# Kernel tuning notes

Hardware: AMD Instinct MI355X
Metric: run time of the kernel (lower is better)

Reference implementation:

```python
import jax, jax.numpy as jnp
import numpy as np

N = 50000       # nodes
E = 400000      # edges (avg degree 8)
IN, HID, OUT, ED = 128, 256, 128, 64
EXP = 2          # GENConv MLP expansion
EPS_MSG = 1e-7   # GENConv eps added to relu(msg)
EPS_BN = 1e-5    # BatchNorm eps
EPS_SM = 1e-16   # PyG softmax denominator eps


def _lin(key, fi, fo):
    w = jax.random.normal(key, (fi, fo), jnp.float32) / np.float32(np.sqrt(fi))
    return w, jnp.zeros((fo,), jnp.float32)


def _layer_params(key, fi, fo, ed):
    ks = jax.random.split(key, 5)
    Wsrc, bsrc = _lin(ks[0], fi, fo)
    Wdst, bdst = _lin(ks[1], fi, fo)
    We, be = _lin(ks[2], ed, fo)
    W1, b1 = _lin(ks[3], fo, fo * EXP)
    W2, b2 = _lin(ks[4], fo * EXP, fo)
    g = jnp.ones((fo * EXP,), jnp.float32)   # BN gamma
    bt = jnp.zeros((fo * EXP,), jnp.float32) # BN beta
    return dict(Wsrc=Wsrc, bsrc=bsrc, Wdst=Wdst, bdst=bdst, We=We, be=be,
                W1=W1, b1=b1, g=g, bt=bt, W2=W2, b2=b2)


def setup_inputs() -> dict:
    key = jax.random.key(0)
    k0, k1, k2, k3, k4 = jax.random.split(key, 5)
    inp = {
        'x': jax.random.normal(k0, (N, IN), jnp.float32),
        'edge_index': jax.random.randint(k1, (2, E), 0, N, jnp.int32),
        'edge_attr': jax.random.normal(k2, (E, ED), jnp.float32),
    }
    for pref, p in (('l1_', _layer_params(k3, IN, HID, ED)),
                    ('l2_', _layer_params(k4, HID, OUT, ED))):
        for n, v in p.items():
            inp[pref + n] = v
    return inp


def _genconv(x, src, dst, ea, Wsrc, bsrc, Wdst, bdst, We, be, W1, b1, g, bt, W2, b2):
    n = x.shape[0]
    h = x @ Wsrc + bsrc                          # [N, F] lin_src
    e = ea @ We + be                             # [E, F] lin_edge
    msg = jax.nn.relu(h[src] + e) + EPS_MSG      # [E, F] message
    # softmax aggregation over destination nodes (t = 1.0)
    mx = jax.ops.segment_max(msg, dst, num_segments=n)
    ex = jnp.exp(msg - mx[dst])
    den = jax.ops.segment_sum(ex, dst, num_segments=n)
    alpha = ex / (den[dst] + EPS_SM)
    agg = jax.ops.segment_sum(alpha * msg, dst, num_segments=n)  # [N, F]
    out = agg + (x @ Wdst + bdst)                # residual lin_dst
    # MLP: Linear -> BatchNorm(train stats) -> ReLU -> Linear
    h1 = out @ W1 + b1                           # [N, 2F]
    mu = h1.mean(0)
    var = h1.var(0)
    h1 = (h1 - mu) * jax.lax.rsqrt(var + EPS_BN) * g + bt
    return jax.nn.relu(h1) @ W2 + b2


def reference(x, edge_index, edge_attr,
              l1_Wsrc, l1_bsrc, l1_Wdst, l1_bdst, l1_We, l1_be,
              l1_W1, l1_b1, l1_g, l1_bt, l1_W2, l1_b2,
              l2_Wsrc, l2_bsrc, l2_Wdst, l2_bdst, l2_We, l2_be,
              l2_W1, l2_b1, l2_g, l2_bt, l2_W2, l2_b2):
    src, dst = edge_index[0], edge_index[1]
    h = _genconv(x, src, dst, edge_attr,
                 l1_Wsrc, l1_bsrc, l1_Wdst, l1_bdst, l1_We, l1_be,
                 l1_W1, l1_b1, l1_g, l1_bt, l1_W2, l1_b2)
    h = jax.nn.relu(h)
    return _genconv(h, src, dst, edge_attr,
                    l2_Wsrc, l2_bsrc, l2_Wdst, l2_bdst, l2_We, l2_be,
                    l2_W1, l2_b1, l2_g, l2_bt, l2_W2, l2_b2)
```

## Files before the change

### kernel.cpp

```cpp
#include <hip/hip_runtime.h>

typedef unsigned short u16;
typedef unsigned int u32;
typedef __attribute__((ext_vector_type(8))) short sv8;
typedef __attribute__((ext_vector_type(4))) float fv4;
typedef __attribute__((ext_vector_type(4))) unsigned short us4;
typedef __attribute__((ext_vector_type(2))) unsigned short us2;

__device__ __forceinline__ u16 f2b(float x) {
    union { float f; u32 u; } a; a.f = x;
    u32 r = a.u + 0x7FFFu + ((a.u >> 16) & 1u);
    return (u16)(r >> 16);
}
__device__ __forceinline__ float b2f(u16 h) {
    union { u32 u; float f; } a; a.u = ((u32)h) << 16;
    return a.f;
}

__device__ __forceinline__ void gll16(const void* g, void* l) {
    __builtin_amdgcn_global_load_lds((__attribute__((address_space(1))) void*)g,
                                     (__attribute__((address_space(3))) void*)l,
                                     16, 0, 0);
}

template<bool AF32, bool AAFF, int EPI, bool STATS>
__global__ __launch_bounds__(256) void k_gemm(
    const void* __restrict__ Aptr, const u16* __restrict__ Wt,
    const float* __restrict__ bias, void* __restrict__ Cptr,
    int M, int K, int F,
    const float* __restrict__ sc, const float* __restrict__ sh,
    float* __restrict__ sums, float* __restrict__ sumsq)
{
    __shared__ u16 As[64][36];
    __shared__ u16 Bs[64][36];
    __shared__ u16 Cs[64][68];
    const int t = threadIdx.x, w = t >> 6, l = t & 63;
    const int n0 = blockIdx.x * 64, m0 = blockIdx.y * 64;
    const int arow = t >> 2, acol = (t & 3) << 3;
    const size_t gr = (size_t)(m0 + arow < M ? m0 + arow : M - 1);

    fv4 acc[4] = {};

    for (int k0 = 0; k0 < K; k0 += 32) {
        sv8 av;
        if constexpr (AF32) {
            const float* Af = (const float*)Aptr;
            fv4 u0 = *(const fv4*)(Af + gr * K + k0 + acol);
            fv4 u1 = *(const fv4*)(Af + gr * K + k0 + acol + 4);
            #pragma unroll
            for (int j = 0; j < 4; ++j) { av[j] = (short)f2b(u0[j]); av[j + 4] = (short)f2b(u1[j]); }
        } else if constexpr (AAFF) {
            sv8 v = *(const sv8*)((const u16*)Aptr + gr * K + k0 + acol);
            fv4 c0 = *(const fv4*)(sc + k0 + acol), c1 = *(const fv4*)(sc + k0 + acol + 4);
            fv4 d0 = *(const fv4*)(sh + k0 + acol), d1 = *(const fv4*)(sh + k0 + acol + 4);
            #pragma unroll
            for (int j = 0; j < 4; ++j) {
                av[j]     = (short)f2b(fmaxf(b2f((u16)v[j])     * c0[j] + d0[j], 0.f));
                av[j + 4] = (short)f2b(fmaxf(b2f((u16)v[j + 4]) * c1[j] + d1[j], 0.f));
            }
        } else {
            av = *(const sv8*)((const u16*)Aptr + gr * K + k0 + acol);
        }
        *(sv8*)&As[arow][acol] = av;
        *(sv8*)&Bs[arow][acol] = *(const sv8*)(Wt + (size_t)(n0 + arow) * K + k0 + acol);
        __syncthreads();

        sv8 a = *(const sv8*)&As[(w << 4) + (l & 15)][(l >> 4) << 3];
        #pragma unroll
        for (int ct = 0; ct < 4; ++ct) {
            sv8 b = *(const sv8*)&Bs[(ct << 4) + (l & 15)][(l >> 4) << 3];
            acc[ct] = __builtin_amdgcn_mfma_f32_16x16x32_bf16(a, b, acc[ct], 0, 0, 0);
        }
        __syncthreads();
    }

    const int lr0 = (w << 4) + ((l >> 4) << 2);
    #pragma unroll
    for (int ct = 0; ct < 4; ++ct) {
        const int col = (ct << 4) + (l & 15);
        const float bv = bias[n0 + col];
        float s = 0.f, s2 = 0.f;
        #pragma unroll
        for (int r = 0; r < 4; ++r) {
            const int lrow = lr0 + r;
            const bool valid = (m0 + lrow) < M;
            float v = acc[ct][r] + bv;
            if constexpr (STATS) { if (valid) { s += v; s2 += v * v; } }
            if constexpr (EPI == 1) v = fmaxf(v, 0.f);
            if constexpr (EPI == 3) {
                if (valid) ((float*)Cptr)[(size_t)(m0 + lrow) * F + n0 + col] = v;
            } else {
                Cs[lrow][col] = f2b(v);
            }
        }
        if constexpr (STATS) {
            s  += __shfl_xor(s, 16);  s  += __shfl_xor(s, 32);
            s2 += __shfl_xor(s2, 16); s2 += __shfl_xor(s2, 32);
            if (l < 16) { unsafeAtomicAdd(&sums[n0 + col], s); unsafeAtomicAdd(&sumsq[n0 + col], s2); }
        }
    }
    if constexpr (EPI != 3) {
        __syncthreads();
        const int lrow = t >> 2, c0 = (t & 3) << 4;
        if (m0 + lrow < M) {
            u16* Cb = (u16*)Cptr + (size_t)(m0 + lrow) * F + n0 + c0;
            *(sv8*)Cb       = *(const sv8*)&Cs[lrow][c0];
            *(sv8*)(Cb + 8) = *(const sv8*)&Cs[lrow][c0 + 8];
        }
    }
}

template<int FN>
__global__ __launch_bounds__(256) void k_egemm(
    const u16* __restrict__ Ab, const u16* __restrict__ Wt,
    const float* __restrict__ bias, u16* __restrict__ Cbuf)
{
    __shared__ u16 smem[4096 + FN * 64];
    u16* As = smem;
    u16* Bs = smem + 4096;
    u16* Cs = Bs;
    const int t = threadIdx.x, w = t >> 6, l = t & 63;
    const int m0 = blockIdx.x * 64;

    #pragma unroll
    for (int i = 0; i < 2; ++i) {
        int slot = ((w * 2 + i) << 6) + l;
        int row = slot >> 3, g = (slot & 7) ^ (row & 7);
        gll16(Ab + (size_t)(m0 + row) * 64 + g * 8, As + ((w * 2 + i) << 6) * 8);
    }
    constexpr int BISS = FN / 32;
    #pragma unroll
    for (int i = 0; i < BISS; ++i) {
        int slot = ((w * BISS + i) << 6) + l;
        int row = slot >> 3, g = (slot & 7) ^ (row & 7);
        gll16(Wt + (size_t)row * 64 + g * 8, Bs + ((w * BISS + i) << 6) * 8);
    }
    __syncthreads();

    const int Arow = (w << 4) + (l & 15);
    const int g0 = l >> 4;
    sv8 a0 = *(const sv8*)&As[(Arow * 8 + ((g0)     ^ (Arow & 7))) * 8];
    sv8 a1 = *(const sv8*)&As[(Arow * 8 + ((g0 + 4) ^ (Arow & 7))) * 8];
    fv4 acc[FN / 16] = {};
    #pragma unroll
    for (int ct = 0; ct < FN / 16; ++ct) {
        int Brow = (ct << 4) + (l & 15);
        sv8 b0 = *(const sv8*)&Bs[(Brow * 8 + ((g0)     ^ (Brow & 7))) * 8];
        sv8 b1 = *(const sv8*)&Bs[(Brow * 8 + ((g0 + 4) ^ (Brow & 7))) * 8];
        acc[ct] = __builtin_amdgcn_mfma_f32_16x16x32_bf16(a0, b0, acc[ct], 0, 0, 0);
        acc[ct] = __builtin_amdgcn_mfma_f32_16x16x32_bf16(a1, b1, acc[ct], 0, 0, 0);
    }
    __syncthreads();

    #pragma unroll
    for (int ct = 0; ct < FN / 16; ++ct) {
        const int col = (ct << 4) + (l & 15);
        const float bv = bias[col];
        #pragma unroll
        for (int r = 0; r < 4; ++r) {
            const int row = (w << 4) + ((l >> 4) << 2) + r;
            int my = (int)f2b(acc[ct][r] + bv);
            int ot = __shfl_xor(my, 1);
            if (!(l & 1)) {
                u32 dw = ((u32)my & 0xFFFFu) | ((u32)ot << 16);
                int gp = (col >> 3) ^ (row & 7);
                ((u32*)Cs)[(row * FN + gp * 8 + (col & 7)) >> 1] = dw;
            }
        }
    }
    __syncthreads();

    const int row = t >> 2;
    #pragma unroll
    for (int i = 0; i < FN / 32; ++i) {
        int g = (t & 3) * (FN / 32) + i;
        int gp = (g & ~7) | ((g & 7) ^ (row & 7));
        sv8 v = *(const sv8*)&Cs[row * FN + gp * 8];
        *(sv8*)(Cbuf + (size_t)(m0 + row) * FN + g * 8) = v;
    }
}

__global__ void k_hist(const int* __restrict__ dst, int* __restrict__ counts, int E) {
    int i = blockIdx.x * 256 + threadIdx.x;
    if (i < E) atomicAdd(&counts[dst[i]], 1);
}

__global__ __launch_bounds__(256) void k_psum(const int* __restrict__ counts,
                                              int* __restrict__ bsum, int n) {
    int i = blockIdx.x * 256 + threadIdx.x;
    int v = (i < n) ? counts[i] : 0;
    #pragma unroll
    for (int o = 1; o < 64; o <<= 1) v += __shfl_xor(v, o);
    __shared__ int ws[4];
    if ((threadIdx.x & 63) == 0) ws[threadIdx.x >> 6] = v;
    __syncthreads();
    if (threadIdx.x == 0) bsum[blockIdx.x] = ws[0] + ws[1] + ws[2] + ws[3];
}

__global__ __launch_bounds__(256) void k_bscan(const int* __restrict__ bsum,
                                               int* __restrict__ boff, int nb) {
    __shared__ int sm[256];
    int t = threadIdx.x;
    int v = (t < nb) ? bsum[t] : 0;
    sm[t] = v; __syncthreads();
    #pragma unroll
    for (int o = 1; o < 256; o <<= 1) {
        int u = (t >= o) ? sm[t - o] : 0;
        __syncthreads();
        sm[t] += u;
        __syncthreads();
    }
    if (t < nb) boff[t] = sm[t] - v;
}

__global__ __launch_bounds__(256) void k_windp(const int* __restrict__ counts,
                                               const int* __restrict__ boff,
                                               int* __restrict__ indptr,
                                               int* __restrict__ cursors, int n) {
    __shared__ int sm[256];
    const int t = threadIdx.x, i = blockIdx.x * 256 + t;
    int v = (i < n) ? counts[i] : 0;
    sm[t] = v; __syncthreads();
    #pragma unroll
    for (int o = 1; o < 256; o <<= 1) {
        int u = (t >= o) ? sm[t - o] : 0;
        __syncthreads();
        sm[t] += u;
        __syncthreads();
    }
    int excl = sm[t] - v + boff[blockIdx.x];
    if (i < n) { indptr[i] = excl; cursors[i] = excl; }
    if (i == n - 1) indptr[n] = excl + v;
}

__global__ void k_scatter(const int* __restrict__ dst, const int* __restrict__ src,
                          int* __restrict__ cursors, int* __restrict__ perm,
                          int* __restrict__ srcp, int E) {
    int i = blockIdx.x * 256 + threadIdx.x;
    if (i < E) {
        int p = atomicAdd(&cursors[dst[i]], 1);
        perm[p] = i;
        srcp[p] = src[i];
    }
}

__global__ __launch_bounds__(256) void k_permea(
    const float* __restrict__ ea, const int* __restrict__ perm,
    u16* __restrict__ eab)
{
    const int t = threadIdx.x;
    const int p = blockIdx.x * 64 + (t >> 2);
    const int q = t & 3;
    const float* srcr = ea + (size_t)perm[p] * 64 + q * 16;
    u16 o[16];
    #pragma unroll
    for (int i = 0; i < 4; ++i) {
        fv4 u = *(const fv4*)(srcr + i * 4);
        o[i * 4 + 0] = f2b(u[0]); o[i * 4 + 1] = f2b(u[1]);
        o[i * 4 + 2] = f2b(u[2]); o[i * 4 + 3] = f2b(u[3]);
    }
    *(sv8*)(eab + (size_t)p * 64 + q * 16)     = *(sv8*)&o[0];
    *(sv8*)(eab + (size_t)p * 64 + q * 16 + 8) = *(sv8*)&o[8];
}

template<int F, int VPT>
__global__ __launch_bounds__(256) void k_agg(
    const u16* __restrict__ e, const u16* __restrict__ hhd,
    const int* __restrict__ srcp, const int* __restrict__ indptr,
    u16* __restrict__ out, int N)
{
    const int nid = blockIdx.x * 4 + (threadIdx.x >> 6);
    if (nid >= N) return;
    const int c0 = (threadIdx.x & 63) * VPT;
    const int S = 2 * F;
    const int p0 = indptr[nid], p1 = indptr[nid + 1];
    float den[VPT] = {}, num[VPT] = {};
    for (int p = p0; p < p1; ++p) {
        const int s = srcp[p];
        u16 ev[VPT], hv[VPT];
        if constexpr (VPT == 4) {
            *(us4*)ev = *(const us4*)&e[(size_t)p * F + c0];
            *(us4*)hv = *(const us4*)&hhd[(size_t)s * S + c0];
        } else {
            *(us2*)ev = *(const us2*)&e[(size_t)p * F + c0];
            *(us2*)hv = *(const us2*)&hhd[(size_t)s * S + c0];
        }
        #pragma unroll
        for (int j = 0; j < VPT; ++j) {
            float x = fmaxf(b2f(ev[j]) + b2f(hv[j]), 0.f) + 1e-7f;
            float ex = __expf(x);
            den[j] += ex;
            num[j] += ex * x;
        }
    }
    #pragma unroll
    for (int j = 0; j < VPT; ++j) {
        float o = num[j] / (den[j] + 1e-16f) + b2f(hhd[(size_t)nid * S + F + c0 + j]);
        out[(size_t)nid * F + c0 + j] = f2b(o);
    }
}

struct WtDesc { const float* W; u16* D; int K; int F; int end; };
struct WtPack { WtDesc d[10]; };

__global__ void k_wtall(WtPack p, int total) {
    int i = blockIdx.x * 256 + threadIdx.x;
    if (i >= total) return;
    int s = 0, base = 0;
    while (i >= p.d[s].end) { base = p.d[s].end; ++s; }
    int loc = i - base;
    int K = p.d[s].K, F = p.d[s].F;
    int f = loc / K, k = loc - f * K;
    p.d[s].D[loc] = f2b(p.d[s].W[(size_t)k * F + f]);
}

__global__ void k_bnfinal(const float* __restrict__ sums, const float* __restrict__ sumsq,
                          const float* __restrict__ g, const float* __restrict__ bt,
                          float* __restrict__ scale, float* __restrict__ shift,
                          int C, float invN)
{
    int c = blockIdx.x * 256 + threadIdx.x;
    if (c < C) {
        float mu  = sums[c] * invN;
        float var = sumsq[c] * invN - mu * mu;
        float s   = g[c] * rsqrtf(var + 1e-5f);
        scale[c] = s;
        shift[c] = bt[c] - mu * s;
    }
}

extern "C" void kernel_launch(void* const* d_in, const int* in_sizes, int n_in,
                              void* d_out, int out_size, void* d_ws, size_t ws_size,
                              hipStream_t stream)
{
    const int IN = 128, HID = 256, OUT = 128, ED = 64;
    const int N = in_sizes[0] / IN;
    const int E = in_sizes[1] / 2;

    const float* x   = (const float*)d_in[0];
    const int*   src = (const int*)d_in[1];
    const int*   dst = src + E;
    const float* ea  = (const float*)d_in[2];
    auto F32 = [&](int i) { return (const float*)d_in[i]; };
    const float *Wsrc1 = F32(3),  *bsrc1 = F32(4),  *Wdst1 = F32(5),  *bdst1 = F32(6),
                *We1   = F32(7),  *be1   = F32(8),  *W11   = F32(9),  *b11   = F32(10),
                *g1    = F32(11), *bt1   = F32(12), *W21   = F32(13), *b21   = F32(14);
    const float *Wsrc2 = F32(15), *bsrc2 = F32(16), *Wdst2 = F32(17), *bdst2 = F32(18),
                *We2   = F32(19), *be2   = F32(20), *W12   = F32(21), *b12   = F32(22),
                *g2    = F32(23), *bt2   = F32(24), *W22   = F32(25), *b22   = F32(26);

    char* wp = (char*)d_ws;
    auto carve = [&](size_t bytes) -> void* {
        void* r = (void*)wp; wp += (bytes + 255) & ~(size_t)255; return r;
    };
    u16* wcat1  = (u16*)carve((size_t)HID * IN * 2);
    u16* wdst1t = (u16*)carve((size_t)HID * IN * 2);
    u16* we1t   = (u16*)carve((size_t)HID * ED * 2);
    u16* w11t   = (u16*)carve((size_t)(2 * HID) * HID * 2);
    u16* w21t   = (u16*)carve((size_t)HID * (2 * HID) * 2);
    u16* wcat2  = (u16*)carve((size_t)OUT * HID * 2);
    u16* wdst2t = (u16*)carve((size_t)OUT * HID * 2);
    u16* we2t   = (u16*)carve((size_t)OUT * ED * 2);
    u16* w12t   = (u16*)carve((size_t)(2 * OUT) * OUT * 2);
    u16* w22t   = (u16*)carve((size_t)OUT * (2 * OUT) * 2);
    int* counts  = (int*)carve((size_t)N * 4);
    int* indptr  = (int*)carve((size_t)(N + 1) * 4);
    int* cursors = (int*)carve((size_t)N * 4);
    int* perm    = (int*)carve((size_t)E * 4);
    int* srcp    = (int*)carve((size_t)E * 4);
    int* bsum    = (int*)carve((size_t)256 * 4);
    int* boff    = (int*)carve((size_t)256 * 4);
    u16* eab  = (u16*)carve((size_t)E * ED * 2);
    u16* hhd  = (u16*)carve((size_t)N * 512 * 2);
    u16* x2   = (u16*)carve((size_t)N * HID * 2);
    u16* ebuf = (u16*)carve((size_t)E * HID * 2);
    float* stats1 = (float*)carve((size_t)1024 * 4);
    float* stats2 = (float*)carve((size_t)512 * 4);
    float* ss1    = (float*)carve((size_t)1024 * 4);
    float* ss2    = (float*)carve((size_t)512 * 4);
    u16* h1 = ebuf;

    hipMemsetAsync(counts, 0, (size_t)N * 4, stream);
    hipMemsetAsync(stats1, 0, (size_t)(1024 + 512) * 4, stream);
    k_hist<<<dim3((E + 255) / 256), dim3(256), 0, stream>>>(dst, counts, E);
    const int nb = (N + 255) / 256;
    k_psum<<<dim3(nb), dim3(256), 0, stream>>>(counts, bsum, N);
    k_bscan<<<dim3(1), dim3(256), 0, stream>>>(bsum, boff, nb);
    k_windp<<<dim3(nb), dim3(256), 0, stream>>>(counts, boff, indptr, cursors, N);
    k_scatter<<<dim3((E + 255) / 256), dim3(256), 0, stream>>>(dst, src, cursors, perm, srcp, E);
    k_permea<<<dim3(E / 64), dim3(256), 0, stream>>>(ea, perm, eab);

    WtPack wpk; int acc_end = 0;
    auto addw = [&](int idx, const float* W, u16* D, int K, int F) {
        acc_end += K * F;
        wpk.d[idx] = WtDesc{W, D, K, F, acc_end};
    };
    addw(0, Wsrc1, wcat1,  IN, HID);   addw(1, Wdst1, wdst1t, IN, HID);
    addw(2, We1,   we1t,   ED, HID);   addw(3, W11,   w11t,   HID, 2 * HID);
    addw(4, W21,   w21t,   2 * HID, HID);
    addw(5, Wsrc2, wcat2,  HID, OUT);  addw(6, Wdst2, wdst2t, HID, OUT);
    addw(7, We2,   we2t,   ED, OUT);   addw(8, W12,   w12t,   OUT, 2 * OUT);
    addw(9, W22,   w22t,   2 * OUT, OUT);
    k_wtall<<<dim3((acc_end + 255) / 256), dim3(256), 0, stream>>>(wpk, acc_end);

    const int gm = (N + 63) / 64;

    float* bcat1 = (float*)carve((size_t)512 * 4);
    float* bcat2 = (float*)carve((size_t)256 * 4);
    hipMemcpyAsync(bcat1,       bsrc1, 256 * 4, hipMemcpyDeviceToDevice, stream);
    hipMemcpyAsync(bcat1 + 256, bdst1, 256 * 4, hipMemcpyDeviceToDevice, stream);
    hipMemcpyAsync(bcat2,       bsrc2, 128 * 4, hipMemcpyDeviceToDevice, stream);
    hipMemcpyAsync(bcat2 + 128, bdst2, 128 * 4, hipMemcpyDeviceToDevice, stream);

    k_gemm<true, false, 0, false><<<dim3(8, gm), dim3(256), 0, stream>>>(
        x, wcat1, bcat1, hhd, N, IN, 512, nullptr, nullptr, nullptr, nullptr);
    k_egemm<256><<<dim3(E / 64), dim3(256), 0, stream>>>(eab, we1t, be1, ebuf);
    k_agg<256, 4><<<dim3((N + 3) / 4), dim3(256), 0, stream>>>(ebuf, hhd, srcp, indptr, x2, N);
    k_gemm<false, false, 0, true><<<dim3(8, gm), dim3(256), 0, stream>>>(
        x2, w11t, b11, h1, N, HID, 512, nullptr, nullptr, stats1, stats1 + 512);
    k_bnfinal<<<dim3(2), dim3(256), 0, stream>>>(
        stats1, stats1 + 512, g1, bt1, ss1, ss1 + 512, 512, 1.f / N);
    k_gemm<false, true, 1, false><<<dim3(4, gm), dim3(256), 0, stream>>>(
        h1, w21t, b21, x2, N, 512, HID, ss1, ss1 + 512, nullptr, nullptr);

    k_gemm<false, false, 0, false><<<dim3(4, gm), dim3(256), 0, stream>>>(
        x2, wcat2, bcat2, hhd, N, HID, 256, nullptr, nullptr, nullptr, nullptr);
    k_egemm<128><<<dim3(E / 64), dim3(256), 0, stream>>>(eab, we2t, be2, ebuf);
    k_agg<128, 2><<<dim3((N + 3) / 4), dim3(256), 0, stream>>>(ebuf, hhd, srcp, indptr, x2, N);
    k_gemm<false, false, 0, true><<<dim3(4, gm), dim3(256), 0, stream>>>(
        x2, w12t, b12, h1, N, OUT, 256, nullptr, nullptr, stats2, stats2 + 256);
    k_bnfinal<<<dim3(1), dim3(256), 0, stream>>>(
        stats2, stats2 + 256, g2, bt2, ss2, ss2 + 256, 256, 1.f / N);
    k_gemm<false, true, 3, false><<<dim3(2, gm), dim3(256), 0, stream>>>(
        h1, w22t, b22, d_out, N, HID, OUT, ss2, ss2 + 256, nullptr, nullptr);
}
```

Before: 746.2 us.

## Fuse edge-attribute permute and bf16 cast into edge GEMM, drop LDS staging

Removes the separate k_permea pass and the bf16 eab buffer. The edge GEMM now gathers fp32 edge_attr rows through perm and converts them to bf16 in registers. The epilogue writes packed bf16 pairs straight to global memory instead of staging through shared memory, and four bias memcpys become one small kernel. This saves a full write and read of the permuted edge array and a launch, but the second layer now re-reads fp32 edge attributes with scattered row access, and the direct stores are less coalesced.

After: 699.9 us. 6.2% less time.

```diff
diff --git a/kernel.cpp b/kernel.cpp
--- a/kernel.cpp
+++ b/kernel.cpp
@@ -111,23 +111,15 @@
 }
 
 template<int FN>
-__global__ __launch_bounds__(256) void k_egemm(
-    const u16* __restrict__ Ab, const u16* __restrict__ Wt,
-    const float* __restrict__ bias, u16* __restrict__ Cbuf)
+__global__ __launch_bounds__(256) void k_egemm3(
+    const float* __restrict__ ea, const int* __restrict__ perm,
+    const u16* __restrict__ Wt, const float* __restrict__ bias,
+    u16* __restrict__ Cbuf)
 {
-    __shared__ u16 smem[4096 + FN * 64];
-    u16* As = smem;
-    u16* Bs = smem + 4096;
-    u16* Cs = Bs;
+    __shared__ u16 Bs[FN * 64];
     const int t = threadIdx.x, w = t >> 6, l = t & 63;
     const int m0 = blockIdx.x * 64;
 
-    #pragma unroll
-    for (int i = 0; i < 2; ++i) {
-        int slot = ((w * 2 + i) << 6) + l;
-        int row = slot >> 3, g = (slot & 7) ^ (row & 7);
-        gll16(Ab + (size_t)(m0 + row) * 64 + g * 8, As + ((w * 2 + i) << 6) * 8);
-    }
     constexpr int BISS = FN / 32;
     #pragma unroll
     for (int i = 0; i < BISS; ++i) {
@@ -135,48 +127,47 @@
         int row = slot >> 3, g = (slot & 7) ^ (row & 7);
         gll16(Wt + (size_t)row * 64 + g * 8, Bs + ((w * BISS + i) << 6) * 8);
     }
+
+    const int g0 = l >> 4;
+    const int gr = m0 + (w << 4) + (l & 15);
+    const int prow = perm[gr];
+    const float* ar = ea + (size_t)prow * 64 + (g0 << 3);
+    fv4 u0 = *(const fv4*)ar;
+    fv4 u1 = *(const fv4*)(ar + 4);
+    fv4 u2 = *(const fv4*)(ar + 32);
+    fv4 u3 = *(const fv4*)(ar + 36);
+    sv8 a0, a1;
+    #pragma unroll
+    for (int j = 0; j < 4; ++j) {
+        a0[j] = (short)f2b(u0[j]); a0[j + 4] = (short)f2b(u1[j]);
+        a1[j] = (short)f2b(u2[j]); a1[j + 4] = (short)f2b(u3[j]);
+    }
     __syncthreads();
 
-    const int Arow = (w << 4) + (l & 15);
-    const int g0 = l >> 4;
-    sv8 a0 = *(const sv8*)&As[(Arow * 8 + ((g0)     ^ (Arow & 7))) * 8];
-    sv8 a1 = *(const sv8*)&As[(Arow * 8 + ((g0 + 4) ^ (Arow & 7))) * 8];
-    fv4 acc[FN / 16] = {};
+    fv4 acc[FN / 16];
     #pragma unroll
     for (int ct = 0; ct < FN / 16; ++ct) {
         int Brow = (ct << 4) + (l & 15);
         sv8 b0 = *(const sv8*)&Bs[(Brow * 8 + ((g0)     ^ (Brow & 7))) * 8];
         sv8 b1 = *(const sv8*)&Bs[(Brow * 8 + ((g0 + 4) ^ (Brow & 7))) * 8];
-        acc[ct] = __builtin_amdgcn_mfma_f32_16x16x32_bf16(a0, b0, acc[ct], 0, 0, 0);
-        acc[ct] = __builtin_amdgcn_mfma_f32_16x16x32_bf16(a1, b1, acc[ct], 0, 0, 0);
-    }
-    __syncthreads();
-
+        fv4 z = {};
+        z = __builtin_amdgcn_mfma_f32_16x16x32_bf16(a0, b0, z, 0, 0, 0);
+        acc[ct] = __builtin_amdgcn_mfma_f32_16x16x32_bf16(a1, b1, z, 0, 0, 0);
+    }
+
+    const int r0 = (w << 4) + ((l >> 4) << 2);
     #pragma unroll
     for (int ct = 0; ct < FN / 16; ++ct) {
         const int col = (ct << 4) + (l & 15);
         const float bv = bias[col];
         #pragma unroll
         for (int r = 0; r < 4; ++r) {
-            const int row = (w << 4) + ((l >> 4) << 2) + r;
-            int my = (int)f2b(acc[ct][r] + bv);
-            int ot = __shfl_xor(my, 1);
-            if (!(l & 1)) {
-                u32 dw = ((u32)my & 0xFFFFu) | ((u32)ot << 16);
-                int gp = (col >> 3) ^ (row & 7);
-                ((u32*)Cs)[(row * FN + gp * 8 + (col & 7)) >> 1] = dw;
-            }
-        }
-    }
-    __syncthreads();
-
-    const int row = t >> 2;
-    #pragma unroll
-    for (int i = 0; i < FN / 32; ++i) {
-        int g = (t & 3) * (FN / 32) + i;
-        int gp = (g & ~7) | ((g & 7) ^ (row & 7));
-        sv8 v = *(const sv8*)&Cs[row * FN + gp * 8];
-        *(sv8*)(Cbuf + (size_t)(m0 + row) * FN + g * 8) = v;
+            const int row = m0 + r0 + r;
+            u32 my = (u32)f2b(acc[ct][r] + bv);
+            u32 ot = (u32)__shfl_xor((int)my, 1);
+            if (!(l & 1))
+                *(u32*)(Cbuf + (size_t)row * FN + col) = (my & 0xFFFFu) | (ot << 16);
+        }
     }
 }
 
@@ -242,25 +233,6 @@
         perm[p] = i;
         srcp[p] = src[i];
     }
-}
-
-__global__ __launch_bounds__(256) void k_permea(
-    const float* __restrict__ ea, const int* __restrict__ perm,
-    u16* __restrict__ eab)
-{
-    const int t = threadIdx.x;
-    const int p = blockIdx.x * 64 + (t >> 2);
-    const int q = t & 3;
-    const float* srcr = ea + (size_t)perm[p] * 64 + q * 16;
-    u16 o[16];
-    #pragma unroll
-    for (int i = 0; i < 4; ++i) {
-        fv4 u = *(const fv4*)(srcr + i * 4);
-        o[i * 4 + 0] = f2b(u[0]); o[i * 4 + 1] = f2b(u[1]);
-        o[i * 4 + 2] = f2b(u[2]); o[i * 4 + 3] = f2b(u[3]);
-    }
-    *(sv8*)(eab + (size_t)p * 64 + q * 16)     = *(sv8*)&o[0];
-    *(sv8*)(eab + (size_t)p * 64 + q * 16 + 8) = *(sv8*)&o[8];
 }
 
 template<int F, int VPT>
@@ -314,6 +286,18 @@
     p.d[s].D[loc] = f2b(p.d[s].W[(size_t)k * F + f]);
 }
 
+__global__ void k_bcat(const float* __restrict__ bsrc1, const float* __restrict__ bdst1,
+                       const float* __restrict__ bsrc2, const float* __restrict__ bdst2,
+                       float* __restrict__ bcat1, float* __restrict__ bcat2) {
+    int t = threadIdx.x;
+    bcat1[t] = bsrc1[t];
+    bcat1[256 + t] = bdst1[t];
+    if (t < 128) {
+        bcat2[t] = bsrc2[t];
+        bcat2[128 + t] = bdst2[t];
+    }
+}
+
 __global__ void k_bnfinal(const float* __restrict__ sums, const float* __restrict__ sumsq,
                           const float* __restrict__ g, const float* __restrict__ bt,
                           float* __restrict__ scale, float* __restrict__ shift,
@@ -370,7 +354,6 @@
     int* srcp    = (int*)carve((size_t)E * 4);
     int* bsum    = (int*)carve((size_t)256 * 4);
     int* boff    = (int*)carve((size_t)256 * 4);
-    u16* eab  = (u16*)carve((size_t)E * ED * 2);
     u16* hhd  = (u16*)carve((size_t)N * 512 * 2);
     u16* x2   = (u16*)carve((size_t)N * HID * 2);
     u16* ebuf = (u16*)carve((size_t)E * HID * 2);
@@ -378,6 +361,8 @@
     float* stats2 = (float*)carve((size_t)512 * 4);
     float* ss1    = (float*)carve((size_t)1024 * 4);
     float* ss2    = (float*)carve((size_t)512 * 4);
+    float* bcat1  = (float*)carve((size_t)512 * 4);
+    float* bcat2  = (float*)carve((size_t)256 * 4);
     u16* h1 = ebuf;
 
     hipMemsetAsync(counts, 0, (size_t)N * 4, stream);
@@ -388,7 +373,6 @@
     k_bscan<<<dim3(1), dim3(256), 0, stream>>>(bsum, boff, nb);
     k_windp<<<dim3(nb), dim3(256), 0, stream>>>(counts, boff, indptr, cursors, N);
     k_scatter<<<dim3((E + 255) / 256), dim3(256), 0, stream>>>(dst, src, cursors, perm, srcp, E);
-    k_permea<<<dim3(E / 64), dim3(256), 0, stream>>>(ea, perm, eab);
 
     WtPack wpk; int acc_end = 0;
     auto addw = [&](int idx, const float* W, u16* D, int K, int F) {
@@ -402,19 +386,13 @@
     addw(7, We2,   we2t,   ED, OUT);   addw(8, W12,   w12t,   OUT, 2 * OUT);
     addw(9, W22,   w22t,   2 * OUT, OUT);
     k_wtall<<<dim3((acc_end + 255) / 256), dim3(256), 0, stream>>>(wpk, acc_end);
+    k_bcat<<<dim3(1), dim3(256), 0, stream>>>(bsrc1, bdst1, bsrc2, bdst2, bcat1, bcat2);
 
     const int gm = (N + 63) / 64;
-
-    float* bcat1 = (float*)carve((size_t)512 * 4);
-    float* bcat2 = (float*)carve((size_t)256 * 4);
-    hipMemcpyAsync(bcat1,       bsrc1, 256 * 4, hipMemcpyDeviceToDevice, stream);
-    hipMemcpyAsync(bcat1 + 256, bdst1, 256 * 4, hipMemcpyDeviceToDevice, stream);
-    hipMemcpyAsync(bcat2,       bsrc2, 128 * 4, hipMemcpyDeviceToDevice, stream);
-    hipMemcpyAsync(bcat2 + 128, bdst2, 128 * 4, hipMemcpyDeviceToDevice, stream);
 
     k_gemm<true, false, 0, false><<<dim3(8, gm), dim3(256), 0, stream>>>(
         x, wcat1, bcat1, hhd, N, IN, 512, nullptr, nullptr, nullptr, nullptr);
-    k_egemm<256><<<dim3(E / 64), dim3(256), 0, stream>>>(eab, we1t, be1, ebuf);
+    k_egemm3<256><<<dim3(E / 64), dim3(256), 0, stream>>>(ea, perm, we1t, be1, ebuf);
     k_agg<256, 4><<<dim3((N + 3) / 4), dim3(256), 0, stream>>>(ebuf, hhd, srcp, indptr, x2, N);
     k_gemm<false, false, 0, true><<<dim3(8, gm), dim3(256), 0, stream>>>(
         x2, w11t, b11, h1, N, HID, 512, nullptr, nullptr, stats1, stats1 + 512);
@@ -425,7 +403,7 @@
 
     k_gemm<false, false, 0, false><<<dim3(4, gm), dim3(256), 0, stream>>>(
         x2, wcat2, bcat2, hhd, N, HID, 256, nullptr, nullptr, nullptr, nullptr);
-    k_egemm<128><<<dim3(E / 64), dim3(256), 0, stream>>>(eab, we2t, be2, ebuf);
+    k_egemm3<128><<<dim3(E / 64), dim3(256), 0, stream>>>(ea, perm, we2t, be2, ebuf);
     k_agg<128, 2><<<dim3((N + 3) / 4), dim3(256), 0, stream>>>(ebuf, hhd, srcp, indptr, x2, N);
     k_gemm<false, false, 0, true><<<dim3(4, gm), dim3(256), 0, stream>>>(
         x2, w12t, b12, h1, N, OUT, 256, nullptr, nullptr, stats2, stats2 + 256);
```
